# Performance work log

Hardware: AMD Instinct MI355X
Metric: run time of the kernel (lower is better)

The kernel has to match this reference:

```python
import jax, jax.numpy as jnp
import numpy as np

N = 50000
E = 600000
FEAT = 32
ACT = 8
H = 128
HEADS = 4
C = H // HEADS
L = 3
NEG_SLOPE = 0.2
LN_EPS = 1e-5


def setup_inputs() -> dict:
    key = jax.random.key(0)
    ks = jax.random.split(key, 32)
    s = 0.05
    inp = {
        'x': jax.random.normal(ks[0], (N, FEAT), jnp.float32),
        'action': jax.random.normal(ks[1], (N, ACT), jnp.float32),
        'edge_index': jax.random.randint(ks[2], (2, E), 0, N, jnp.int32),
        # node encoder: Linear(feat+act -> H) + LayerNorm
        'W0': jax.random.normal(ks[3], (FEAT + ACT, H), jnp.float32) * s,
        'b0': jnp.zeros((H,), jnp.float32),
        'ln0_g': jnp.ones((H,), jnp.float32),
        'ln0_b': jnp.zeros((H,), jnp.float32),
        # GAT layers (stacked over L): lin W [L,H,heads*C], att vectors, bias, LayerNorm
        'Wg': jax.random.normal(ks[4], (L, H, HEADS * C), jnp.float32) * s,
        'att_src': jax.random.normal(ks[5], (L, HEADS, C), jnp.float32) * s,
        'att_dst': jax.random.normal(ks[6], (L, HEADS, C), jnp.float32) * s,
        'bg': jnp.zeros((L, HEADS * C), jnp.float32),
        'lng_g': jnp.ones((L, H), jnp.float32),
        'lng_b': jnp.zeros((L, H), jnp.float32),
        # dynamics head
        'Wd1': jax.random.normal(ks[7], (H, H), jnp.float32) * s,
        'bd1': jnp.zeros((H,), jnp.float32),
        'Wd2': jax.random.normal(ks[8], (H, FEAT), jnp.float32) * s,
        'bd2': jnp.zeros((FEAT,), jnp.float32),
        # reward head
        'Wr1': jax.random.normal(ks[9], (H, H // 2), jnp.float32) * s,
        'br1': jnp.zeros((H // 2,), jnp.float32),
        'Wr2': jax.random.normal(ks[10], (H // 2, 1), jnp.float32) * s,
        'br2': jnp.zeros((1,), jnp.float32),
        # constraint head
        'Wc1': jax.random.normal(ks[11], (H, H // 2), jnp.float32) * s,
        'bc1': jnp.zeros((H // 2,), jnp.float32),
        'Wc2': jax.random.normal(ks[12], (H // 2, 1), jnp.float32) * s,
        'bc2': jnp.zeros((1,), jnp.float32),
    }
    return inp


def _layernorm(x, g, b):
    mu = jnp.mean(x, axis=-1, keepdims=True)
    var = jnp.mean(jnp.square(x - mu), axis=-1, keepdims=True)
    return (x - mu) * jax.lax.rsqrt(var + LN_EPS) * g + b


def _gat_layer(h, src, dst, W, a_src, a_dst, bias):
    # PyG GATConv: xp = lin(h) per head; alpha = leaky_relu(a_src.x_j + a_dst.x_i)
    xp = (h @ W).reshape(N, HEADS, C)                    # [N, heads, C]
    s_src = jnp.sum(xp * a_src, axis=-1)                 # [N, heads]
    s_dst = jnp.sum(xp * a_dst, axis=-1)                 # [N, heads]
    alpha = jax.nn.leaky_relu(s_src[src] + s_dst[dst], NEG_SLOPE)  # [E', heads]
    # segment softmax over edges grouped by destination node
    amax = jax.ops.segment_max(alpha, dst, num_segments=N)
    ex = jnp.exp(alpha - amax[dst])
    den = jax.ops.segment_sum(ex, dst, num_segments=N)
    attn = ex / den[dst]                                 # [E', heads]
    msg = xp[src] * attn[..., None]                      # [E', heads, C]
    out = jax.ops.segment_sum(msg.reshape(-1, HEADS * C), dst, num_segments=N)
    return out + bias                                    # [N, H]


def reference(x, action, edge_index, W0, b0, ln0_g, ln0_b, Wg, att_src, att_dst,
              bg, lng_g, lng_b, Wd1, bd1, Wd2, bd2, Wr1, br1, Wr2, br2,
              Wc1, bc1, Wc2, bc2):
    # add self loops (PyG GATConv default)
    loops = jnp.arange(N, dtype=edge_index.dtype)
    src = jnp.concatenate([edge_index[0], loops])
    dst = jnp.concatenate([edge_index[1], loops])

    h = jax.nn.relu(_layernorm(jnp.concatenate([x, action], axis=-1) @ W0 + b0, ln0_g, ln0_b))
    for l in range(L):
        h_new = _gat_layer(h, src, dst, Wg[l], att_src[l], att_dst[l], bg[l])
        h_new = jax.nn.relu(_layernorm(h_new, lng_g[l], lng_b[l]))
        h = h + h_new

    delta_x = jax.nn.relu(h @ Wd1 + bd1) @ Wd2 + bd2
    next_x = x + delta_x
    graph_emb = jnp.mean(h, axis=0, keepdims=True)       # global_mean_pool, single graph
    reward = (jax.nn.relu(graph_emb @ Wr1 + br1) @ Wr2 + br2).squeeze(-1)
    constraint_prob = jax.nn.sigmoid(jax.nn.relu(graph_emb @ Wc1 + bc1) @ Wc2 + bc2).squeeze(-1)
    return delta_x, next_x, reward, constraint_prob
```

## Files before the change

kernel.cpp:

```cpp
#include <hip/hip_runtime.h>

typedef unsigned short u16;
typedef __attribute__((ext_vector_type(8))) short bf16x8;
typedef __attribute__((ext_vector_type(4))) float f32x4;

#define NN 50000
#define EE 600000
#define EP 650000
#define LNEPS 1e-5f
#define NB 196
#define ENCB 1563
#define HB 2344
#define CNTB 2540

__device__ __forceinline__ float bf2f(u16 u) {
    union { unsigned int i; float f; } v; v.i = ((unsigned int)u) << 16; return v.f;
}
__device__ __forceinline__ u16 f2bf(float f) {
    union { float f; unsigned int i; } v; v.f = f;
    unsigned int x = v.i;
    unsigned int r = x + 0x7fffu + ((x >> 16) & 1u);
    return (u16)(r >> 16);
}
__device__ __forceinline__ float ldf(const void* p, long i, int bf) {
    return bf ? bf2f(((const u16*)p)[i]) : ((const float*)p)[i];
}
__device__ __forceinline__ void stf(void* p, long i, int bf, float v) {
    if (bf) ((u16*)p)[i] = f2bf(v); else ((float*)p)[i] = v;
}

#define WTOT 93858
#define BSWN 65536
struct P22 { const void* p[22]; };

__global__ __launch_bounds__(256) void init8(P22 w, float* __restrict__ wf,
                                             u16* __restrict__ bsw,
                                             int* __restrict__ deg8,
                                             float* __restrict__ gacc,
                                             int* __restrict__ flag) {
    const unsigned w0 = *(const unsigned*)w.p[2];
    const int bf = (w0 == 0x3F803F80u) ? 1 : 0;
    int i = blockIdx.x * 256 + threadIdx.x;
    if (i < WTOT) {
        const int offs[23] = {0,5120,5248,5376,5504,54656,55040,55424,55808,56192,56576,
                              72960,73088,77184,77216,85408,85472,85536,85537,93729,93793,
                              93857,93858};
        int seg = 0;
        while (offs[seg + 1] <= i) ++seg;
        wf[i] = ldf(w.p[seg], i - offs[seg], bf);
        return;
    }
    i -= WTOT;
    if (i < BSWN) {
        int mat = i >> 14, rem = i & 16383;
        int ct = rem >> 11, r2 = rem & 2047;
        int kb = r2 >> 9, r3 = r2 & 511;
        int lane = r3 >> 3, j = r3 & 7;
        int k = kb * 32 + (lane >> 4) * 8 + j;
        int n = ct * 16 + (lane & 15);
        float v = (mat < 3) ? ldf(w.p[4], (long)mat * 16384 + (long)k * 128 + n, bf)
                            : ldf(w.p[10], (long)k * 128 + n, bf);
        bsw[i] = f2bf(v);
        return;
    }
    i -= BSWN;
    if (i < NN * 8) { deg8[i] = 0; return; }
    i -= NN * 8;
    if (i < 2048) { gacc[i] = 0.f; return; }
    if (i == 2048) *flag = bf;
}

__global__ __launch_bounds__(256) void enc9(
    const void* __restrict__ x, const void* __restrict__ act,
    const float* __restrict__ wf, u16* __restrict__ hb,
    const int* __restrict__ flg, const int* __restrict__ ei,
    int* __restrict__ deg8, int* __restrict__ rank) {
    if (blockIdx.x >= ENCB) {
        int hbk = blockIdx.x - ENCB;
        int e = hbk * 256 + threadIdx.x;
        if (e < EE) {
            int d = ei[EE + e];
            int rep = hbk & 7;
            rank[e] = atomicAdd(&deg8[d * 8 + rep], 1);
        }
        return;
    }
    const float* W0f = wf;
    const float* b0f = wf + 5120;
    const float* gf  = wf + 5248;
    const float* bbf = wf + 5376;
    __shared__ float As[32][41];
    const int bf = *flg;
    int t = threadIdx.x;
    int r0 = blockIdx.x * 32;
    #pragma unroll
    for (int i = 0; i < 5; ++i) {
        int idx = t + i * 256;
        int r = idx / 40, k = idx - r * 40;
        int rr = r0 + r; if (rr >= NN) rr = NN - 1;
        As[r][k] = (k < 32) ? ldf(x, (long)rr * 32 + k, bf)
                            : ldf(act, (long)rr * 8 + (k - 32), bf);
    }
    __syncthreads();
    int colq = t & 31, mq = t >> 5;
    int col0 = colq * 4;
    float4 b0v = *(const float4*)(b0f + col0);
    float acc[4][4];
    #pragma unroll
    for (int j = 0; j < 4; ++j) {
        acc[j][0] = b0v.x; acc[j][1] = b0v.y; acc[j][2] = b0v.z; acc[j][3] = b0v.w;
    }
    #pragma unroll 2
    for (int k = 0; k < 40; ++k) {
        float4 b4 = *(const float4*)(W0f + k * 128 + col0);
        float a0 = As[mq * 4 + 0][k];
        float a1 = As[mq * 4 + 1][k];
        float a2 = As[mq * 4 + 2][k];
        float a3 = As[mq * 4 + 3][k];
        acc[0][0] += a0 * b4.x; acc[0][1] += a0 * b4.y; acc[0][2] += a0 * b4.z; acc[0][3] += a0 * b4.w;
        acc[1][0] += a1 * b4.x; acc[1][1] += a1 * b4.y; acc[1][2] += a1 * b4.z; acc[1][3] += a1 * b4.w;
        acc[2][0] += a2 * b4.x; acc[2][1] += a2 * b4.y; acc[2][2] += a2 * b4.z; acc[2][3] += a2 * b4.w;
        acc[3][0] += a3 * b4.x; acc[3][1] += a3 * b4.y; acc[3][2] += a3 * b4.z; acc[3][3] += a3 * b4.w;
    }
    float4 gv = *(const float4*)(gf + col0);
    float4 bv = *(const float4*)(bbf + col0);
    #pragma unroll
    for (int j = 0; j < 4; ++j) {
        int row = r0 + mq * 4 + j;
        float pa = acc[j][0] + acc[j][1] + acc[j][2] + acc[j][3];
        #pragma unroll
        for (int o = 1; o <= 16; o <<= 1) pa += __shfl_xor(pa, o, 32);
        float mu = pa * (1.f / 128.f);
        float d0 = acc[j][0] - mu, d1 = acc[j][1] - mu;
        float d2 = acc[j][2] - mu, d3 = acc[j][3] - mu;
        float q = d0 * d0 + d1 * d1 + d2 * d2 + d3 * d3;
        #pragma unroll
        for (int o = 1; o <= 16; o <<= 1) q += __shfl_xor(q, o, 32);
        float rs = rsqrtf(q * (1.f / 128.f) + LNEPS);
        if (row < NN) {
            ushort4 hbv;
            hbv.x = f2bf(fmaxf(d0 * rs * gv.x + bv.x, 0.f));
            hbv.y = f2bf(fmaxf(d1 * rs * gv.y + bv.y, 0.f));
            hbv.z = f2bf(fmaxf(d2 * rs * gv.z + bv.z, 0.f));
            hbv.w = f2bf(fmaxf(d3 * rs * gv.w + bv.w, 0.f));
            *(ushort4*)(hb + (long)row * 128 + col0) = hbv;
        }
    }
}

__global__ __launch_bounds__(256) void scanA2(const int* __restrict__ deg8,
                                              int* __restrict__ bsum) {
    __shared__ int red[256];
    int t = threadIdx.x; int i = blockIdx.x * 256 + t;
    int s = 0;
    if (i < NN) {
        int4 lo = *(const int4*)(deg8 + (long)i * 8);
        int4 hi = *(const int4*)(deg8 + (long)i * 8 + 4);
        s = lo.x + lo.y + lo.z + lo.w + hi.x + hi.y + hi.z + hi.w + 1;
    }
    red[t] = s; __syncthreads();
    for (int s2 = 128; s2 >= 1; s2 >>= 1) { if (t < s2) red[t] += red[t + s2]; __syncthreads(); }
    if (t == 0) bsum[blockIdx.x] = red[0];
}

__global__ __launch_bounds__(256) void scanC4(const int* __restrict__ deg8,
                                              const int* __restrict__ bsum,
                                              int* __restrict__ offs,
                                              int* __restrict__ repOff8) {
    __shared__ int sh[256];
    int t = threadIdx.x;
    sh[t] = (t < NB) ? bsum[t] : 0;
    __syncthreads();
    for (int o = 1; o < 256; o <<= 1) {
        int u = (t >= o) ? sh[t - o] : 0;
        __syncthreads();
        sh[t] += u;
        __syncthreads();
    }
    int pre = (blockIdx.x == 0) ? 0 : sh[blockIdx.x - 1];
    __syncthreads();
    int i = blockIdx.x * 256 + t;
    int c[8]; int v = 0;
    if (i < NN) {
        int4 lo = *(const int4*)(deg8 + (long)i * 8);
        int4 hi = *(const int4*)(deg8 + (long)i * 8 + 4);
        c[0] = lo.x; c[1] = lo.y; c[2] = lo.z; c[3] = lo.w;
        c[4] = hi.x; c[5] = hi.y; c[6] = hi.z; c[7] = hi.w;
        v = c[0] + c[1] + c[2] + c[3] + c[4] + c[5] + c[6] + c[7] + 1;
    }
    sh[t] = v;
    __syncthreads();
    for (int o = 1; o < 256; o <<= 1) {
        int u = (t >= o) ? sh[t - o] : 0;
        __syncthreads();
        sh[t] += u;
        __syncthreads();
    }
    if (i < NN) {
        offs[i] = pre + sh[t] - v;
        int rp[8]; int run = 0;
        #pragma unroll
        for (int r2 = 0; r2 < 8; ++r2) { rp[r2] = run; run += c[r2]; }
        int4 v0; v0.x = rp[0]; v0.y = rp[1]; v0.z = rp[2]; v0.w = rp[3];
        int4 v1; v1.x = rp[4]; v1.y = rp[5]; v1.z = rp[6]; v1.w = rp[7];
        *(int4*)(repOff8 + (long)i * 8) = v0;
        *(int4*)(repOff8 + (long)i * 8 + 4) = v1;
    }
    if (i == 0) offs[NN] = EP;
}

__global__ __launch_bounds__(256) void lin_score(
    const u16* __restrict__ hb, const u16* __restrict__ bswm,
    u16* __restrict__ out, const float* __restrict__ wf, int layer,
    float* __restrict__ s_src, float* __restrict__ s_dst,
    int doscatter, const int* __restrict__ ei, const int* __restrict__ rank,
    const int* __restrict__ offs, const int* __restrict__ repOff8,
    int* __restrict__ csrc) {
    if (doscatter && blockIdx.x >= ENCB) {
        int e = (blockIdx.x - ENCB) * 256 + threadIdx.x;
        if (e < EP) {
            if (e < EE) {
                int sv = ei[e], d = ei[EE + e];
                int rep = (e >> 8) & 7;
                csrc[offs[d] + repOff8[(long)d * 8 + rep] + rank[e]] = sv;
            } else {
                int n = e - EE;
                csrc[offs[n + 1] - 1] = n;
            }
        }
        return;
    }
    __shared__ u16 As[32 * 136];
    int t = threadIdx.x;
    int r0 = blockIdx.x * 32;
    #pragma unroll
    for (int i = 0; i < 2; ++i) {
        int idx = (t + i * 256) * 8;
        int r = idx >> 7, k = idx & 127;
        int rr = r0 + r; if (rr >= NN) rr = NN - 1;
        int4 v = *(const int4*)(hb + (long)rr * 128 + k);
        *(int4*)(As + r * 136 + k) = v;
    }
    __syncthreads();
    int w = t >> 6, lane = t & 63;
    int rt = w & 1, ctbase = (w >> 1) * 4;
    int quad = lane >> 4, l15 = lane & 15;
    int rowl = rt * 16 + l15;
    bf16x8 afr[4];
    #pragma unroll
    for (int kb = 0; kb < 4; ++kb)
        afr[kb] = *(const bf16x8*)(As + rowl * 136 + kb * 32 + quad * 8);
    const float* asrf = wf + 54656 + layer * 128;
    const float* adsf = wf + 55040 + layer * 128;
    int headbase = (w >> 1) * 2;
    #pragma unroll
    for (int cp = 0; cp < 2; ++cp) {
        int ct0 = ctbase + cp * 2, ct1 = ct0 + 1;
        f32x4 acc0 = {0.f, 0.f, 0.f, 0.f};
        f32x4 acc1 = {0.f, 0.f, 0.f, 0.f};
        #pragma unroll
        for (int kb = 0; kb < 4; ++kb) {
            bf16x8 b0 = *(const bf16x8*)(bswm + ct0 * 2048 + kb * 512 + lane * 8);
            acc0 = __builtin_amdgcn_mfma_f32_16x16x32_bf16(afr[kb], b0, acc0, 0, 0, 0);
        }
        #pragma unroll
        for (int kb = 0; kb < 4; ++kb) {
            bf16x8 b1 = *(const bf16x8*)(bswm + ct1 * 2048 + kb * 512 + lane * 8);
            acc1 = __builtin_amdgcn_mfma_f32_16x16x32_bf16(afr[kb], b1, acc1, 0, 0, 0);
        }
        int col0 = ct0 * 16 + l15, col1 = ct1 * 16 + l15;
        #pragma unroll
        for (int reg = 0; reg < 4; ++reg) {
            int grow = r0 + rt * 16 + quad * 4 + reg;
            if (grow < NN) {
                out[(long)grow * 128 + col0] = f2bf(acc0[reg]);
                out[(long)grow * 128 + col1] = f2bf(acc1[reg]);
            }
        }
        float av0 = asrf[col0], av1 = asrf[col1];
        float dv0 = adsf[col0], dv1 = adsf[col1];
        #pragma unroll
        for (int reg = 0; reg < 4; ++reg) {
            float pa = acc0[reg] * av0 + acc1[reg] * av1;
            float pb = acc0[reg] * dv0 + acc1[reg] * dv1;
            #pragma unroll
            for (int o = 1; o <= 8; o <<= 1) {
                pa += __shfl_xor(pa, o, 64);
                pb += __shfl_xor(pb, o, 64);
            }
            if (l15 == 0) {
                int grow = r0 + rt * 16 + quad * 4 + reg;
                if (grow < NN) {
                    s_src[grow * 4 + headbase + cp] = pa;
                    s_dst[grow * 4 + headbase + cp] = pb;
                }
            }
        }
    }
}

__global__ __launch_bounds__(256) void lin_final(
    const u16* __restrict__ hb, const u16* __restrict__ bswm,
    const float* __restrict__ wf, const void* __restrict__ x,
    void* __restrict__ dout, const int* __restrict__ flg,
    float* __restrict__ gacc) {
    __shared__ u16 As[32 * 136];
    __shared__ u16 ts[32 * 136];
    __shared__ float ps[128];
    const float* bias = wf + 72960;
    int t = threadIdx.x;
    int r0 = blockIdx.x * 32;
    #pragma unroll
    for (int i = 0; i < 2; ++i) {
        int idx = (t + i * 256) * 8;
        int r = idx >> 7, k = idx & 127;
        int rr = r0 + r; if (rr >= NN) rr = NN - 1;
        int4 v = *(const int4*)(hb + (long)rr * 128 + k);
        *(int4*)(As + r * 136 + k) = v;
    }
    __syncthreads();
    int w = t >> 6, lane = t & 63;
    int rt = w & 1, ctbase = (w >> 1) * 4;
    int quad = lane >> 4, l15 = lane & 15;
    int rowl = rt * 16 + l15;
    bf16x8 afr[4];
    #pragma unroll
    for (int kb = 0; kb < 4; ++kb)
        afr[kb] = *(const bf16x8*)(As + rowl * 136 + kb * 32 + quad * 8);
    #pragma unroll
    for (int cp = 0; cp < 2; ++cp) {
        int ct0 = ctbase + cp * 2, ct1 = ct0 + 1;
        f32x4 acc0 = {0.f, 0.f, 0.f, 0.f};
        f32x4 acc1 = {0.f, 0.f, 0.f, 0.f};
        #pragma unroll
        for (int kb = 0; kb < 4; ++kb) {
            bf16x8 b0 = *(const bf16x8*)(bswm + ct0 * 2048 + kb * 512 + lane * 8);
            acc0 = __builtin_amdgcn_mfma_f32_16x16x32_bf16(afr[kb], b0, acc0, 0, 0, 0);
        }
        #pragma unroll
        for (int kb = 0; kb < 4; ++kb) {
            bf16x8 b1 = *(const bf16x8*)(bswm + ct1 * 2048 + kb * 512 + lane * 8);
            acc1 = __builtin_amdgcn_mfma_f32_16x16x32_bf16(afr[kb], b1, acc1, 0, 0, 0);
        }
        int col0 = ct0 * 16 + l15, col1 = ct1 * 16 + l15;
        float bia0 = bias[col0], bia1 = bias[col1];
        #pragma unroll
        for (int reg = 0; reg < 4; ++reg) {
            int lrow = rt * 16 + quad * 4 + reg;
            ts[lrow * 136 + col0] = f2bf(fmaxf(acc0[reg] + bia0, 0.f));
            ts[lrow * 136 + col1] = f2bf(fmaxf(acc1[reg] + bia1, 0.f));
        }
    }
    __syncthreads();
    const float* Wd2f = wf + 73088;
    const float* bd2f = wf + 77184;
    const int bf = *flg;
    int c = t & 31, mq = t >> 5;
    float acc[4];
    #pragma unroll
    for (int j = 0; j < 4; ++j) acc[j] = bd2f[c];
    #pragma unroll 4
    for (int k = 0; k < 128; ++k) {
        float wv = Wd2f[k * 32 + c];
        acc[0] += bf2f(ts[(mq * 4 + 0) * 136 + k]) * wv;
        acc[1] += bf2f(ts[(mq * 4 + 1) * 136 + k]) * wv;
        acc[2] += bf2f(ts[(mq * 4 + 2) * 136 + k]) * wv;
        acc[3] += bf2f(ts[(mq * 4 + 3) * 136 + k]) * wv;
    }
    #pragma unroll
    for (int j = 0; j < 4; ++j) {
        int node = r0 + mq * 4 + j;
        if (node >= NN) continue;
        stf(dout, (long)node * 32 + c, bf, acc[j]);
        stf(dout, (long)NN * 32 + (long)node * 32 + c, bf,
            ldf(x, (long)node * 32 + c, bf) + acc[j]);
    }
    int pc = t & 127, half = t >> 7;
    float s = 0.f;
    #pragma unroll
    for (int r2 = half * 16; r2 < half * 16 + 16; ++r2) {
        if (r0 + r2 < NN) s += bf2f(As[r2 * 136 + pc]);
    }
    if (half == 0) ps[pc] = s;
    __syncthreads();
    if (half == 1) atomicAdd(&gacc[(blockIdx.x & 15) * 128 + pc], s + ps[pc]);
}

__global__ __launch_bounds__(128) void head5(
    const float* __restrict__ gacc, const float* __restrict__ wf,
    void* __restrict__ out, const int* __restrict__ flg) {
    const float* Wr1f = wf + 77216;
    const float* br1f = wf + 85408;
    const float* Wr2f = wf + 85472;
    const float* br2f = wf + 85536;
    const float* Wc1f = wf + 85537;
    const float* bc1f = wf + 93729;
    const float* Wc2f = wf + 93793;
    const float* bc2f = wf + 93857;
    __shared__ float ge[128];
    __shared__ float hr[128];
    const int bf = *flg;
    int t = threadIdx.x;
    {
        float s = 0.f;
        #pragma unroll
        for (int k2 = 0; k2 < 16; ++k2) s += gacc[k2 * 128 + t];
        ge[t] = s * (1.f / (float)NN);
    }
    __syncthreads();
    {
        int j = t & 63;
        const float* W = (t < 64) ? Wr1f : Wc1f;
        const float* bb = (t < 64) ? br1f : bc1f;
        float a = bb[j];
        for (int k = 0; k < 128; ++k) a += ge[k] * W[k * 64 + j];
        hr[t] = fmaxf(a, 0.f);
    }
    __syncthreads();
    if (t == 0) {
        float r = br2f[0];
        for (int j = 0; j < 64; ++j) r += hr[j] * Wr2f[j];
        stf(out, (long)2 * NN * 32, bf, r);
    } else if (t == 1) {
        float z = bc2f[0];
        for (int j = 0; j < 64; ++j) z += hr[64 + j] * Wc2f[j];
        float p = 1.f / (1.f + __expf(-z));
        stf(out, (long)2 * NN * 32 + 1, bf, p);
    }
}

__global__ __launch_bounds__(256) void agg10(
    const u16* __restrict__ xp, const float* __restrict__ s_src,
    const float* __restrict__ s_dst,
    const int* __restrict__ csrc, const int* __restrict__ offs,
    const float* __restrict__ wf, int layer, u16* __restrict__ hb) {
    const float* bgf = wf + 55424 + layer * 128;
    const float* gf  = wf + 55808 + layer * 128;
    const float* bbf = wf + 56192 + layer * 128;
    int t = threadIdx.x;
    int lane = t & 63;
    int n = blockIdx.x * 4 + (t >> 6);
    int q = (lane >> 4) & 3;
    int l16 = lane & 15;
    int c0 = l16 * 8;
    int hd = l16 >> 2;
    long idx0 = (long)n * 128 + c0;
    int4 hold = *(const int4*)(hb + idx0);
    float sdn = s_dst[n * 4 + (lane & 3)];
    int beg = offs[n], end = offs[n + 1];
    float a[8] = {};
    float den = 0.f;
    for (int cbeg = beg; cbeg < end; cbeg += 64) {
        int cdeg = end - cbeg; if (cdeg > 64) cdeg = 64;
        int eidx = (lane < cdeg) ? csrc[cbeg + lane] : n;
        for (int base = 0; base < cdeg; base += 16) {
            int me = base + (lane >> 2);
            int sm = __shfl(eidx, me & 63, 64);
            float aw = s_src[sm * 4 + (lane & 3)] + sdn;
            aw = (aw > 0.f) ? aw : 0.2f * aw;
            float wv = (me < cdeg) ? __expf(aw) : 0.f;
            int s00 = __shfl(eidx, base + q, 64);
            int s01 = __shfl(eidx, base + 4 + q, 64);
            int s10 = __shfl(eidx, base + 8 + q, 64);
            int s11 = __shfl(eidx, base + 12 + q, 64);
            int4 v00 = *(const int4*)(xp + (long)s00 * 128 + c0);
            int4 v01 = *(const int4*)(xp + (long)s01 * 128 + c0);
            int4 v10 = *(const int4*)(xp + (long)s10 * 128 + c0);
            int4 v11 = *(const int4*)(xp + (long)s11 * 128 + c0);
            float w00 = __shfl(wv, (q << 2) | hd, 64);
            float w01 = __shfl(wv, ((4 + q) << 2) | hd, 64);
            float w10 = __shfl(wv, ((8 + q) << 2) | hd, 64);
            float w11 = __shfl(wv, ((12 + q) << 2) | hd, 64);
            union { int4 i; u16 u[8]; } u00, u01, u10, u11;
            u00.i = v00; u01.i = v01; u10.i = v10; u11.i = v11;
            #pragma unroll
            for (int k = 0; k < 8; ++k)
                a[k] += w00 * bf2f(u00.u[k]) + w01 * bf2f(u01.u[k])
                      + w10 * bf2f(u10.u[k]) + w11 * bf2f(u11.u[k]);
            den += w00 + w01 + w10 + w11;
        }
    }
    #pragma unroll
    for (int k = 0; k < 8; ++k) {
        a[k] += __shfl_xor(a[k], 16, 64);
        a[k] += __shfl_xor(a[k], 32, 64);
    }
    den += __shfl_xor(den, 16, 64);
    den += __shfl_xor(den, 32, 64);
    float inv = 1.f / den;
    float4 bg0 = *(const float4*)(bgf + c0);
    float4 bg1 = *(const float4*)(bgf + c0 + 4);
    float v[8];
    v[0] = a[0] * inv + bg0.x; v[1] = a[1] * inv + bg0.y;
    v[2] = a[2] * inv + bg0.z; v[3] = a[3] * inv + bg0.w;
    v[4] = a[4] * inv + bg1.x; v[5] = a[5] * inv + bg1.y;
    v[6] = a[6] * inv + bg1.z; v[7] = a[7] * inv + bg1.w;
    float pa = v[0] + v[1] + v[2] + v[3] + v[4] + v[5] + v[6] + v[7];
    #pragma unroll
    for (int o = 1; o <= 8; o <<= 1) pa += __shfl_xor(pa, o, 16);
    float mu = pa * (1.f / 128.f);
    float d[8];
    float qv = 0.f;
    #pragma unroll
    for (int k = 0; k < 8; ++k) { d[k] = v[k] - mu; qv += d[k] * d[k]; }
    #pragma unroll
    for (int o = 1; o <= 8; o <<= 1) qv += __shfl_xor(qv, o, 16);
    float rs = rsqrtf(qv * (1.f / 128.f) + LNEPS);
    float4 g0 = *(const float4*)(gf + c0);
    float4 g1 = *(const float4*)(gf + c0 + 4);
    float4 b0 = *(const float4*)(bbf + c0);
    float4 b1 = *(const float4*)(bbf + c0 + 4);
    float gg[8]  = {g0.x, g0.y, g0.z, g0.w, g1.x, g1.y, g1.z, g1.w};
    float bbv[8] = {b0.x, b0.y, b0.z, b0.w, b1.x, b1.y, b1.z, b1.w};
    if (lane < 16) {
        union { int4 i; u16 u[8]; } hv, ho;
        ho.i = hold;
        #pragma unroll
        for (int k = 0; k < 8; ++k) {
            float y = fmaxf(d[k] * rs * gg[k] + bbv[k], 0.f);
            hv.u[k] = f2bf(bf2f(ho.u[k]) + y);
        }
        *(int4*)(hb + idx0) = hv.i;
    }
}

extern "C" void kernel_launch(void* const* d_in, const int* in_sizes, int n_in,
                              void* d_out, int out_size, void* d_ws, size_t ws_size,
                              hipStream_t stream) {
    const void* x   = d_in[0];
    const void* act = d_in[1];
    const int*  ei  = (const int*)d_in[2];

    char* ws = (char*)d_ws;
    size_t off = 0;
    auto alloc = [&](size_t bytes) -> char* {
        char* p = ws + off;
        off = (off + bytes + 255) & ~(size_t)255;
        return p;
    };
    u16*       hb      = (u16*)   alloc((size_t)NN * 128 * 2);
    u16*       xp      = (u16*)   alloc((size_t)NN * 128 * 2);
    float*     s_src   = (float*) alloc((size_t)NN * 4 * 4);
    float*     s_dst   = (float*) alloc((size_t)NN * 4 * 4);
    int*       deg8    = (int*)   alloc((size_t)NN * 8 * 4);
    int*       rank    = (int*)   alloc((size_t)EE * 4);
    int*       offs    = (int*)   alloc((size_t)(NN + 1) * 4);
    int*       repOff8 = (int*)   alloc((size_t)NN * 8 * 4);
    int*       csrc    = (int*)   alloc((size_t)EP * 4);
    float*     wf      = (float*) alloc((size_t)WTOT * 4);
    u16*       bsw     = (u16*)   alloc((size_t)BSWN * 2);
    float*     gacc    = (float*) alloc(16 * 128 * 4);
    int*       flag    = (int*)   alloc(4);
    int*       bsum    = (int*)   alloc((size_t)NB * 4);

    P22 wp;
    for (int i = 0; i < 22; ++i) wp.p[i] = d_in[3 + i];
    const int initN = WTOT + BSWN + NN * 8 + 2048 + 1;
    init8<<<(initN + 255) / 256, 256, 0, stream>>>(wp, wf, bsw, deg8, gacc, flag);

    enc9<<<ENCB + HB, 256, 0, stream>>>(x, act, wf, hb, flag, ei, deg8, rank);

    scanA2<<<NB, 256, 0, stream>>>(deg8, bsum);
    scanC4<<<NB, 256, 0, stream>>>(deg8, bsum, offs, repOff8);

    for (int l = 0; l < 3; ++l) {
        int grid = (l == 0) ? (ENCB + CNTB) : ENCB;
        lin_score<<<grid, 256, 0, stream>>>(hb, bsw + (size_t)l * 16384, xp,
                                            wf, l, s_src, s_dst,
                                            (l == 0) ? 1 : 0, ei, rank, offs,
                                            repOff8, csrc);
        agg10<<<NN / 4, 256, 0, stream>>>(xp, s_src, s_dst, csrc, offs,
                                          wf, l, hb);
    }

    lin_final<<<ENCB, 256, 0, stream>>>(hb, bsw + (size_t)3 * 16384,
                                        wf, x, d_out, flag, gacc);

    head5<<<1, 128, 0, stream>>>(gacc, wf, d_out, flag);

    (void)in_sizes; (void)n_in; (void)out_size; (void)ws_size;
}
```

Baseline: 356.9 us.

## Fuse weight conversion into encoder and simplify CSR degree counting and scan

Moves weight conversion and swizzling out of the init kernel and into extra blocks of the encoder kernel, which now reads raw weights directly. Replaces the 8-way replicated degree counters with a single counter per node, so the two-pass scan becomes one kernel that recomputes each block's prefix by summing all earlier degrees. This cuts one kernel launch and the replicated counter and offset traffic, at the cost of more atomic contention on one counter per node and quadratic prefix work in the scan.

```diff
diff --git a/kernel.cpp b/kernel.cpp
--- a/kernel.cpp
+++ b/kernel.cpp
@@ -12,6 +12,9 @@
 #define ENCB 1563
 #define HB 2344
 #define CNTB 2540
+#define WTOT 93858
+#define BSWN 65536
+#define WCVB 624
 
 __device__ __forceinline__ float bf2f(u16 u) {
     union { unsigned int i; float f; } v; v.i = ((unsigned int)u) << 16; return v.f;
@@ -29,70 +32,65 @@
     if (bf) ((u16*)p)[i] = f2bf(v); else ((float*)p)[i] = v;
 }
 
-#define WTOT 93858
-#define BSWN 65536
 struct P22 { const void* p[22]; };
 
-__global__ __launch_bounds__(256) void init8(P22 w, float* __restrict__ wf,
-                                             u16* __restrict__ bsw,
-                                             int* __restrict__ deg8,
+__global__ __launch_bounds__(256) void init9(const void* __restrict__ g0p,
+                                             int* __restrict__ deg,
                                              float* __restrict__ gacc,
                                              int* __restrict__ flag) {
-    const unsigned w0 = *(const unsigned*)w.p[2];
-    const int bf = (w0 == 0x3F803F80u) ? 1 : 0;
     int i = blockIdx.x * 256 + threadIdx.x;
-    if (i < WTOT) {
-        const int offs[23] = {0,5120,5248,5376,5504,54656,55040,55424,55808,56192,56576,
-                              72960,73088,77184,77216,85408,85472,85536,85537,93729,93793,
-                              93857,93858};
-        int seg = 0;
-        while (offs[seg + 1] <= i) ++seg;
-        wf[i] = ldf(w.p[seg], i - offs[seg], bf);
+    if (i < NN) { deg[i] = 0; return; }
+    i -= NN;
+    if (i < 2048) { gacc[i] = 0.f; return; }
+    if (i == 2048) *flag = (*(const unsigned*)g0p == 0x3F803F80u) ? 1 : 0;
+}
+
+__global__ __launch_bounds__(256) void enc10(
+    const void* __restrict__ x, const void* __restrict__ act,
+    const int* __restrict__ ei, P22 w,
+    u16* __restrict__ hb, int* __restrict__ deg, int* __restrict__ rank,
+    float* __restrict__ wf, u16* __restrict__ bsw) {
+    const int bf = (*(const unsigned*)w.p[2] == 0x3F803F80u) ? 1 : 0;
+    int b = blockIdx.x, t = threadIdx.x;
+    if (b >= ENCB + HB) {
+        int i = (b - ENCB - HB) * 256 + t;
+        if (i < WTOT) {
+            const int offs[23] = {0,5120,5248,5376,5504,54656,55040,55424,55808,56192,56576,
+                                  72960,73088,77184,77216,85408,85472,85536,85537,93729,93793,
+                                  93857,93858};
+            int seg = 0;
+            while (offs[seg + 1] <= i) ++seg;
+            wf[i] = ldf(w.p[seg], i - offs[seg], bf);
+            return;
+        }
+        i -= WTOT;
+        if (i < BSWN) {
+            int mat = i >> 14, rem = i & 16383;
+            int ct = rem >> 11, r2 = rem & 2047;
+            int kb = r2 >> 9, r3 = r2 & 511;
+            int lane = r3 >> 3, j = r3 & 7;
+            int k = kb * 32 + (lane >> 4) * 8 + j;
+            int n = ct * 16 + (lane & 15);
+            float v = (mat < 3) ? ldf(w.p[4], (long)mat * 16384 + (long)k * 128 + n, bf)
+                                : ldf(w.p[10], (long)k * 128 + n, bf);
+            bsw[i] = f2bf(v);
+        }
         return;
     }
-    i -= WTOT;
-    if (i < BSWN) {
-        int mat = i >> 14, rem = i & 16383;
-        int ct = rem >> 11, r2 = rem & 2047;
-        int kb = r2 >> 9, r3 = r2 & 511;
-        int lane = r3 >> 3, j = r3 & 7;
-        int k = kb * 32 + (lane >> 4) * 8 + j;
-        int n = ct * 16 + (lane & 15);
-        float v = (mat < 3) ? ldf(w.p[4], (long)mat * 16384 + (long)k * 128 + n, bf)
-                            : ldf(w.p[10], (long)k * 128 + n, bf);
-        bsw[i] = f2bf(v);
-        return;
-    }
-    i -= BSWN;
-    if (i < NN * 8) { deg8[i] = 0; return; }
-    i -= NN * 8;
-    if (i < 2048) { gacc[i] = 0.f; return; }
-    if (i == 2048) *flag = bf;
-}
-
-__global__ __launch_bounds__(256) void enc9(
-    const void* __restrict__ x, const void* __restrict__ act,
-    const float* __restrict__ wf, u16* __restrict__ hb,
-    const int* __restrict__ flg, const int* __restrict__ ei,
-    int* __restrict__ deg8, int* __restrict__ rank) {
-    if (blockIdx.x >= ENCB) {
-        int hbk = blockIdx.x - ENCB;
-        int e = hbk * 256 + threadIdx.x;
+    if (b >= ENCB) {
+        int e = (b - ENCB) * 256 + t;
         if (e < EE) {
             int d = ei[EE + e];
-            int rep = hbk & 7;
-            rank[e] = atomicAdd(&deg8[d * 8 + rep], 1);
+            rank[e] = atomicAdd(&deg[d], 1);
         }
         return;
     }
-    const float* W0f = wf;
-    const float* b0f = wf + 5120;
-    const float* gf  = wf + 5248;
-    const float* bbf = wf + 5376;
+    const void* W0p = w.p[0];
+    const void* b0p = w.p[1];
+    const void* g0p = w.p[2];
+    const void* bb0p = w.p[3];
     __shared__ float As[32][41];
-    const int bf = *flg;
-    int t = threadIdx.x;
-    int r0 = blockIdx.x * 32;
+    int r0 = b * 32;
     #pragma unroll
     for (int i = 0; i < 5; ++i) {
         int idx = t + i * 256;
@@ -104,26 +102,34 @@
     __syncthreads();
     int colq = t & 31, mq = t >> 5;
     int col0 = colq * 4;
-    float4 b0v = *(const float4*)(b0f + col0);
     float acc[4][4];
-    #pragma unroll
-    for (int j = 0; j < 4; ++j) {
-        acc[j][0] = b0v.x; acc[j][1] = b0v.y; acc[j][2] = b0v.z; acc[j][3] = b0v.w;
+    {
+        float b0 = ldf(b0p, col0, bf), b1 = ldf(b0p, col0 + 1, bf);
+        float b2 = ldf(b0p, col0 + 2, bf), b3 = ldf(b0p, col0 + 3, bf);
+        #pragma unroll
+        for (int j = 0; j < 4; ++j) {
+            acc[j][0] = b0; acc[j][1] = b1; acc[j][2] = b2; acc[j][3] = b3;
+        }
     }
     #pragma unroll 2
     for (int k = 0; k < 40; ++k) {
-        float4 b4 = *(const float4*)(W0f + k * 128 + col0);
+        float w0 = ldf(W0p, (long)k * 128 + col0, bf);
+        float w1 = ldf(W0p, (long)k * 128 + col0 + 1, bf);
+        float w2 = ldf(W0p, (long)k * 128 + col0 + 2, bf);
+        float w3 = ldf(W0p, (long)k * 128 + col0 + 3, bf);
         float a0 = As[mq * 4 + 0][k];
         float a1 = As[mq * 4 + 1][k];
         float a2 = As[mq * 4 + 2][k];
         float a3 = As[mq * 4 + 3][k];
-        acc[0][0] += a0 * b4.x; acc[0][1] += a0 * b4.y; acc[0][2] += a0 * b4.z; acc[0][3] += a0 * b4.w;
-        acc[1][0] += a1 * b4.x; acc[1][1] += a1 * b4.y; acc[1][2] += a1 * b4.z; acc[1][3] += a1 * b4.w;
-        acc[2][0] += a2 * b4.x; acc[2][1] += a2 * b4.y; acc[2][2] += a2 * b4.z; acc[2][3] += a2 * b4.w;
-        acc[3][0] += a3 * b4.x; acc[3][1] += a3 * b4.y; acc[3][2] += a3 * b4.z; acc[3][3] += a3 * b4.w;
-    }
-    float4 gv = *(const float4*)(gf + col0);
-    float4 bv = *(const float4*)(bbf + col0);
+        acc[0][0] += a0 * w0; acc[0][1] += a0 * w1; acc[0][2] += a0 * w2; acc[0][3] += a0 * w3;
+        acc[1][0] += a1 * w0; acc[1][1] += a1 * w1; acc[1][2] += a1 * w2; acc[1][3] += a1 * w3;
+        acc[2][0] += a2 * w0; acc[2][1] += a2 * w1; acc[2][2] += a2 * w2; acc[2][3] += a2 * w3;
+        acc[3][0] += a3 * w0; acc[3][1] += a3 * w1; acc[3][2] += a3 * w2; acc[3][3] += a3 * w3;
+    }
+    float gv0 = ldf(g0p, col0, bf), gv1 = ldf(g0p, col0 + 1, bf);
+    float gv2 = ldf(g0p, col0 + 2, bf), gv3 = ldf(g0p, col0 + 3, bf);
+    float bv0 = ldf(bb0p, col0, bf), bv1 = ldf(bb0p, col0 + 1, bf);
+    float bv2 = ldf(bb0p, col0 + 2, bf), bv3 = ldf(bb0p, col0 + 3, bf);
     #pragma unroll
     for (int j = 0; j < 4; ++j) {
         int row = r0 + mq * 4 + j;
@@ -139,74 +145,35 @@
         float rs = rsqrtf(q * (1.f / 128.f) + LNEPS);
         if (row < NN) {
             ushort4 hbv;
-            hbv.x = f2bf(fmaxf(d0 * rs * gv.x + bv.x, 0.f));
-            hbv.y = f2bf(fmaxf(d1 * rs * gv.y + bv.y, 0.f));
-            hbv.z = f2bf(fmaxf(d2 * rs * gv.z + bv.z, 0.f));
-            hbv.w = f2bf(fmaxf(d3 * rs * gv.w + bv.w, 0.f));
+            hbv.x = f2bf(fmaxf(d0 * rs * gv0 + bv0, 0.f));
+            hbv.y = f2bf(fmaxf(d1 * rs * gv1 + bv1, 0.f));
+            hbv.z = f2bf(fmaxf(d2 * rs * gv2 + bv2, 0.f));
+            hbv.w = f2bf(fmaxf(d3 * rs * gv3 + bv3, 0.f));
             *(ushort4*)(hb + (long)row * 128 + col0) = hbv;
         }
     }
 }
 
-__global__ __launch_bounds__(256) void scanA2(const int* __restrict__ deg8,
-                                              int* __restrict__ bsum) {
-    __shared__ int red[256];
-    int t = threadIdx.x; int i = blockIdx.x * 256 + t;
+__global__ __launch_bounds__(256) void scan1(const int* __restrict__ deg,
+                                             int* __restrict__ offs) {
+    __shared__ int sh[256];
+    int b = blockIdx.x, t = threadIdx.x;
+    int lim = b * 256;
     int s = 0;
-    if (i < NN) {
-        int4 lo = *(const int4*)(deg8 + (long)i * 8);
-        int4 hi = *(const int4*)(deg8 + (long)i * 8 + 4);
-        s = lo.x + lo.y + lo.z + lo.w + hi.x + hi.y + hi.z + hi.w + 1;
-    }
-    red[t] = s; __syncthreads();
-    for (int s2 = 128; s2 >= 1; s2 >>= 1) { if (t < s2) red[t] += red[t + s2]; __syncthreads(); }
-    if (t == 0) bsum[blockIdx.x] = red[0];
-}
-
-__global__ __launch_bounds__(256) void scanC4(const int* __restrict__ deg8,
-                                              const int* __restrict__ bsum,
-                                              int* __restrict__ offs,
-                                              int* __restrict__ repOff8) {
-    __shared__ int sh[256];
-    int t = threadIdx.x;
-    sh[t] = (t < NB) ? bsum[t] : 0;
-    __syncthreads();
+    for (int i2 = t; i2 < lim; i2 += 256) s += deg[i2];
+    sh[t] = s; __syncthreads();
+    for (int o = 128; o >= 1; o >>= 1) { if (t < o) sh[t] += sh[t + o]; __syncthreads(); }
+    int pre = sh[0] + lim;
+    __syncthreads();
+    int i = lim + t;
+    int v = (i < NN) ? (deg[i] + 1) : 0;
+    sh[t] = v; __syncthreads();
     for (int o = 1; o < 256; o <<= 1) {
         int u = (t >= o) ? sh[t - o] : 0;
-        __syncthreads();
-        sh[t] += u;
-        __syncthreads();
-    }
-    int pre = (blockIdx.x == 0) ? 0 : sh[blockIdx.x - 1];
-    __syncthreads();
-    int i = blockIdx.x * 256 + t;
-    int c[8]; int v = 0;
-    if (i < NN) {
-        int4 lo = *(const int4*)(deg8 + (long)i * 8);
-        int4 hi = *(const int4*)(deg8 + (long)i * 8 + 4);
-        c[0] = lo.x; c[1] = lo.y; c[2] = lo.z; c[3] = lo.w;
-        c[4] = hi.x; c[5] = hi.y; c[6] = hi.z; c[7] = hi.w;
-        v = c[0] + c[1] + c[2] + c[3] + c[4] + c[5] + c[6] + c[7] + 1;
-    }
-    sh[t] = v;
-    __syncthreads();
-    for (int o = 1; o < 256; o <<= 1) {
-        int u = (t >= o) ? sh[t - o] : 0;
-        __syncthreads();
-        sh[t] += u;
-        __syncthreads();
-    }
-    if (i < NN) {
-        offs[i] = pre + sh[t] - v;
-        int rp[8]; int run = 0;
-        #pragma unroll
-        for (int r2 = 0; r2 < 8; ++r2) { rp[r2] = run; run += c[r2]; }
-        int4 v0; v0.x = rp[0]; v0.y = rp[1]; v0.z = rp[2]; v0.w = rp[3];
-        int4 v1; v1.x = rp[4]; v1.y = rp[5]; v1.z = rp[6]; v1.w = rp[7];
-        *(int4*)(repOff8 + (long)i * 8) = v0;
-        *(int4*)(repOff8 + (long)i * 8 + 4) = v1;
-    }
-    if (i == 0) offs[NN] = EP;
+        __syncthreads(); sh[t] += u; __syncthreads();
+    }
+    if (i < NN) offs[i] = pre + sh[t] - v;
+    if (b == 0 && t == 0) offs[NN] = EP;
 }
 
 __global__ __launch_bounds__(256) void lin_score(
@@ -214,15 +181,13 @@
     u16* __restrict__ out, const float* __restrict__ wf, int layer,
     float* __restrict__ s_src, float* __restrict__ s_dst,
     int doscatter, const int* __restrict__ ei, const int* __restrict__ rank,
-    const int* __restrict__ offs, const int* __restrict__ repOff8,
-    int* __restrict__ csrc) {
+    const int* __restrict__ offs, int* __restrict__ csrc) {
     if (doscatter && blockIdx.x >= ENCB) {
         int e = (blockIdx.x - ENCB) * 256 + threadIdx.x;
         if (e < EP) {
             if (e < EE) {
                 int sv = ei[e], d = ei[EE + e];
-                int rep = (e >> 8) & 7;
-                csrc[offs[d] + repOff8[(long)d * 8 + rep] + rank[e]] = sv;
+                csrc[offs[d] + rank[e]] = sv;
             } else {
                 int n = e - EE;
                 csrc[offs[n + 1] - 1] = n;
@@ -538,37 +503,35 @@
         off = (off + bytes + 255) & ~(size_t)255;
         return p;
     };
-    u16*       hb      = (u16*)   alloc((size_t)NN * 128 * 2);
-    u16*       xp      = (u16*)   alloc((size_t)NN * 128 * 2);
-    float*     s_src   = (float*) alloc((size_t)NN * 4 * 4);
-    float*     s_dst   = (float*) alloc((size_t)NN * 4 * 4);
-    int*       deg8    = (int*)   alloc((size_t)NN * 8 * 4);
-    int*       rank    = (int*)   alloc((size_t)EE * 4);
-    int*       offs    = (int*)   alloc((size_t)(NN + 1) * 4);
-    int*       repOff8 = (int*)   alloc((size_t)NN * 8 * 4);
-    int*       csrc    = (int*)   alloc((size_t)EP * 4);
-    float*     wf      = (float*) alloc((size_t)WTOT * 4);
-    u16*       bsw     = (u16*)   alloc((size_t)BSWN * 2);
-    float*     gacc    = (float*) alloc(16 * 128 * 4);
-    int*       flag    = (int*)   alloc(4);
-    int*       bsum    = (int*)   alloc((size_t)NB * 4);
+    u16*       hb     = (u16*)   alloc((size_t)NN * 128 * 2);
+    u16*       xp     = (u16*)   alloc((size_t)NN * 128 * 2);
+    float*     s_src  = (float*) alloc((size_t)NN * 4 * 4);
+    float*     s_dst  = (float*) alloc((size_t)NN * 4 * 4);
+    int*       deg    = (int*)   alloc((size_t)NN * 4);
+    int*       rank   = (int*)   alloc((size_t)EE * 4);
+    int*       offs   = (int*)   alloc((size_t)(NN + 1) * 4);
+    int*       csrc   = (int*)   alloc((size_t)EP * 4);
+    float*     wf     = (float*) alloc((size_t)WTOT * 4);
+    u16*       bsw    = (u16*)   alloc((size_t)BSWN * 2);
+    float*     gacc   = (float*) alloc(16 * 128 * 4);
+    int*       flag   = (int*)   alloc(4);
 
     P22 wp;
     for (int i = 0; i < 22; ++i) wp.p[i] = d_in[3 + i];
-    const int initN = WTOT + BSWN + NN * 8 + 2048 + 1;
-    init8<<<(initN + 255) / 256, 256, 0, stream>>>(wp, wf, bsw, deg8, gacc, flag);
-
-    enc9<<<ENCB + HB, 256, 0, stream>>>(x, act, wf, hb, flag, ei, deg8, rank);
-
-    scanA2<<<NB, 256, 0, stream>>>(deg8, bsum);
-    scanC4<<<NB, 256, 0, stream>>>(deg8, bsum, offs, repOff8);
+
+    init9<<<(NN + 2048 + 1 + 255) / 256, 256, 0, stream>>>(d_in[5], deg, gacc, flag);
+
+    enc10<<<ENCB + HB + WCVB, 256, 0, stream>>>(x, act, ei, wp, hb, deg, rank,
+                                                wf, bsw);
+
+    scan1<<<NB, 256, 0, stream>>>(deg, offs);
 
     for (int l = 0; l < 3; ++l) {
         int grid = (l == 0) ? (ENCB + CNTB) : ENCB;
         lin_score<<<grid, 256, 0, stream>>>(hb, bsw + (size_t)l * 16384, xp,
                                             wf, l, s_src, s_dst,
                                             (l == 0) ? 1 : 0, ei, rank, offs,
-                                            repOff8, csrc);
+                                            csrc);
         agg10<<<NN / 4, 256, 0, stream>>>(xp, s_src, s_dst, csrc, offs,
                                           wf, l, hb);
     }
```

After: 419.0 us. 17.4% more time.
